# Kernel optimization log

Hardware: AMD Instinct MI355X
Metric: run time of the kernel (lower is better)

The kernel has to match this reference:

```python
import jax, jax.numpy as jnp
import numpy as np

N, D, H, L = 2048, 768, 12, 3
WL, DPE, E = 8, 16, 32768
DFF = 4 * D
EPS = 1e-5


def _ln(x, g, b):
    m = jnp.mean(x, axis=-1, keepdims=True)
    v = jnp.mean(jnp.square(x - m), axis=-1, keepdims=True)
    return (x - m) * jax.lax.rsqrt(v + EPS) * g + b


def setup_inputs() -> dict:
    key = jax.random.key(0)
    ks = jax.random.split(key, 20)
    s = 0.02
    return {
        "node_features": jax.random.normal(ks[0], (N, D), jnp.float32),
        "edge_index": jax.random.randint(ks[1], (2, E), 0, N, jnp.int32),
        "W_rwpe": jax.random.normal(ks[2], (WL, DPE), jnp.float32) * s,
        "b_rwpe": jnp.zeros((DPE,), jnp.float32),
        "Wqkv": jax.random.normal(ks[3], (L, D, 3 * D), jnp.float32) * s,
        "bqkv": jnp.zeros((L, 3 * D), jnp.float32),
        "Wpe": jax.random.normal(ks[4], (L, DPE, H), jnp.float32) * s,
        "bpe": jnp.zeros((L, H), jnp.float32),
        "Wout": jax.random.normal(ks[5], (L, D, D), jnp.float32) * s,
        "bout": jnp.zeros((L, D), jnp.float32),
        "W1": jax.random.normal(ks[6], (L, D, DFF), jnp.float32) * s,
        "b1": jnp.zeros((L, DFF), jnp.float32),
        "W2": jax.random.normal(ks[7], (L, DFF, D), jnp.float32) * s,
        "b2": jnp.zeros((L, D), jnp.float32),
        "g1": jnp.ones((L, D), jnp.float32),
        "beta1": jnp.zeros((L, D), jnp.float32),
        "g2": jnp.ones((L, D), jnp.float32),
        "beta2": jnp.zeros((L, D), jnp.float32),
    }


def _rw_pe(edge_index, W_rwpe, b_rwpe):
    # symmetrized adjacency with duplicate-edge summation (matches coalesce)
    src, tgt = edge_index[0], edge_index[1]
    rows = jnp.concatenate([src, tgt])
    cols = jnp.concatenate([tgt, src])
    A = jnp.zeros((N, N), jnp.float32).at[rows, cols].add(1.0)
    deg = jnp.clip(jnp.sum(A, axis=1), 1.0, None)
    T = A / deg[:, None]
    diags = []
    Tk = T
    for k in range(WL):
        diags.append(jnp.diagonal(Tk))
        if k < WL - 1:
            Tk = Tk @ T
    rw = jnp.stack(diags, axis=1)  # [N, WL]
    return rw @ W_rwpe + b_rwpe  # [N, DPE]


def _forward(node_features, edge_index, W_rwpe, b_rwpe, Wqkv, bqkv, Wpe, bpe,
             Wout, bout, W1, b1, W2, b2, g1, beta1, g2, beta2):
    pe = _rw_pe(edge_index, W_rwpe, b_rwpe)
    hd = D // H
    scale = hd ** -0.5
    h = node_features
    for l in range(L):
        qkv = (h @ Wqkv[l] + bqkv[l]).reshape(N, 3, H, hd)
        q, k, v = qkv[:, 0], qkv[:, 1], qkv[:, 2]  # [N, H, hd]
        pp = pe @ Wpe[l] + bpe[l]  # [N, H]
        # bias[h_, i, j] = pp[j, h_] - pp[i, h_]
        bias = (pp[None, :, :] - pp[:, None, :]).transpose(2, 0, 1)
        scores = jnp.einsum('ihd,jhd->hij', q, k) * scale + bias
        attn = jax.nn.softmax(scores, axis=-1)
        out = jnp.einsum('hij,jhd->ihd', attn, v).reshape(N, D)
        out = out @ Wout[l] + bout[l]
        h = _ln(h + out, g1[l], beta1[l])
        f = jax.nn.gelu(h @ W1[l] + b1[l], approximate=False) @ W2[l] + b2[l]
        h = _ln(h + f, g2[l], beta2[l])
    return h


def reference(node_features, edge_index, W_rwpe, b_rwpe, Wqkv, bqkv, Wpe, bpe,
              Wout, bout, W1, b1, W2, b2, g1, beta1, g2, beta2):
    return _forward(node_features, edge_index, W_rwpe, b_rwpe, Wqkv, bqkv,
                    Wpe, bpe, Wout, bout, W1, b1, W2, b2, g1, beta1, g2, beta2)
```

## Files before the change

kernel.cpp:

```cpp
#include <hip/hip_runtime.h>
#include <math.h>

#define NN 2048
#define EE 32768
#define CAP 256

typedef __attribute__((ext_vector_type(8))) short bf16x8;
typedef __attribute__((ext_vector_type(4))) float f32x4;
typedef __attribute__((ext_vector_type(8))) unsigned short u16x8;
typedef __attribute__((ext_vector_type(4))) unsigned short u16x4;

__device__ inline unsigned short f2bu(float x){
  unsigned u = __builtin_bit_cast(unsigned, x);
  return (unsigned short)((u + 0x7fffu + ((u>>16)&1u)) >> 16);
}
__device__ inline float bu2f(unsigned short h){
  unsigned u = ((unsigned)h) << 16;
  return __builtin_bit_cast(float, u);
}
__device__ inline int swz8(int row, int kg){ return row*32 + ((kg ^ ((row>>1)&3))<<3); }
__device__ inline int swzA(int row, int kg){ return row*64 + ((kg ^ (row&7))<<3); }


__global__ __launch_bounds__(256) void scatter_edges(const int* __restrict__ ei, float* __restrict__ A){
  int e = blockIdx.x*256 + threadIdx.x;
  if (e >= EE) return;
  int s = ei[e], t = ei[EE + e];
  atomicAdd(&A[(size_t)s*NN + t], 1.0f);
  atomicAdd(&A[(size_t)t*NN + s], 1.0f);
}

__global__ __launch_bounds__(256) void row_norm(float* __restrict__ A, float* __restrict__ rw){
  __shared__ float sbuf[4];
  int i = blockIdx.x, t = threadIdx.x;
  float s = 0.f;
  for (int m = t; m < NN; m += 256) s += A[(size_t)i*NN + m];
  for (int w = 32; w >= 1; w >>= 1) s += __shfl_xor(s, w, 64);
  if ((t & 63) == 0) sbuf[t >> 6] = s;
  __syncthreads();
  s = sbuf[0] + sbuf[1] + sbuf[2] + sbuf[3];
  float inv = 1.0f / fmaxf(s, 1.0f);
  for (int m = t; m < NN; m += 256){
    float v = A[(size_t)i*NN + m] * inv;
    A[(size_t)i*NN + m] = v;
    if (m == i) rw[i*8 + 0] = v;
  }
}

__global__ __launch_bounds__(256) void build_csc(const float* __restrict__ T, float* __restrict__ cscv,
                                                 int* __restrict__ cscm, int* __restrict__ cnt){
  __shared__ int scnt;
  int j = blockIdx.x, t = threadIdx.x;
  if (t == 0) scnt = 0;
  __syncthreads();
  for (int m = t; m < NN; m += 256){
    float tv = T[(size_t)j*NN + m];
    if (tv != 0.f){
      int p = atomicAdd(&scnt, 1);
      if (p < CAP){
        cscm[j*CAP + p] = m;
        cscv[j*CAP + p] = T[(size_t)m*NN + j];
      }
    }
  }
  __syncthreads();
  if (t == 0) cnt[j] = min(scnt, CAP);
}

__global__ __launch_bounds__(256) void spmm4(const float* __restrict__ Tk, const float* __restrict__ cscv,
                                             const int* __restrict__ cscm, const int* __restrict__ cnt,
                                             float* __restrict__ Tn, float* __restrict__ rw, int kidx){
  __shared__ float tk[4][NN + 4];
  int i0 = blockIdx.x*4, t = threadIdx.x;
  for (int r = 0; r < 4; r++){
    for (int m4 = t; m4 < NN/4; m4 += 256){
      float4 v = *(const float4*)&Tk[(size_t)(i0+r)*NN + m4*4];
      tk[r][m4*4+0] = v.x; tk[r][m4*4+1] = v.y; tk[r][m4*4+2] = v.z; tk[r][m4*4+3] = v.w;
    }
  }
  __syncthreads();
  for (int j = t; j < NN; j += 256){
    int n = cnt[j];
    const int*   im = &cscm[j*CAP];
    const float* iv = &cscv[j*CAP];
    float a0=0.f,a1=0.f,a2=0.f,a3=0.f;
    for (int c = 0; c < n; c++){
      int m = im[c]; float v = iv[c];
      a0 += v*tk[0][m]; a1 += v*tk[1][m]; a2 += v*tk[2][m]; a3 += v*tk[3][m];
    }
    Tn[(size_t)(i0+0)*NN + j] = a0;
    Tn[(size_t)(i0+1)*NN + j] = a1;
    Tn[(size_t)(i0+2)*NN + j] = a2;
    Tn[(size_t)(i0+3)*NN + j] = a3;
    if (j == i0+0) rw[j*8 + kidx] = a0;
    if (j == i0+1) rw[j*8 + kidx] = a1;
    if (j == i0+2) rw[j*8 + kidx] = a2;
    if (j == i0+3) rw[j*8 + kidx] = a3;
  }
}

__global__ __launch_bounds__(256) void pe_kernel(const float* __restrict__ rw, const float* __restrict__ W,
                                                 const float* __restrict__ b, float* __restrict__ pe){
  int idx = blockIdx.x*256 + threadIdx.x;
  if (idx >= NN*16) return;
  int i = idx >> 4, c = idx & 15;
  float acc = b[c];
  #pragma unroll
  for (int k = 0; k < 8; k++) acc += rw[i*8+k] * W[k*16+c];
  pe[idx] = acc;
}

__global__ __launch_bounds__(256) void pp_kernel(const float* __restrict__ pe, const float* __restrict__ Wpe,
                                                 const float* __restrict__ bpe, float* __restrict__ pp){
  int idx = blockIdx.x*256 + threadIdx.x;
  if (idx >= 3*NN*12) return;
  int l = idx / (NN*12);
  int rm = idx % (NN*12);
  int j = rm / 12, h = rm % 12;
  float acc = bpe[l*12 + h];
  #pragma unroll
  for (int c = 0; c < 16; c++) acc += pe[j*16+c] * Wpe[(l*16+c)*12 + h];
  pp[idx] = acc;
}

__global__ __launch_bounds__(256) void wconv(const float* __restrict__ W, unsigned short* __restrict__ Thi,
                                             unsigned short* __restrict__ Tlo, int K, int N){
  __shared__ float ld[32*33];
  int k0 = blockIdx.y*32, n0 = blockIdx.x*32;
  int t = threadIdx.x;
  int r = t>>3, c4 = (t&7)*4;
  float4 v = *(const float4*)&W[(size_t)(k0+r)*N + n0 + c4];
  ld[(c4+0)*33 + r] = v.x; ld[(c4+1)*33 + r] = v.y; ld[(c4+2)*33 + r] = v.z; ld[(c4+3)*33 + r] = v.w;
  __syncthreads();
  u16x4 hi, lo;
  #pragma unroll
  for (int i = 0; i < 4; i++){
    float x = ld[r*33 + c4 + i];
    unsigned short hh = f2bu(x);
    hi[i] = hh;
    lo[i] = f2bu(x - bu2f(hh));
  }
  *(u16x4*)&Thi[(size_t)(n0+r)*K + k0 + c4] = hi;
  *(u16x4*)&Tlo[(size_t)(n0+r)*K + k0 + c4] = lo;
}

template<int DOGELU, int MREP, int NREP>
__global__ __launch_bounds__(256) void gemm_mfma(const float* __restrict__ A,
    const unsigned short* __restrict__ BThi, const unsigned short* __restrict__ BTlo,
    const float* __restrict__ bias, float* __restrict__ C, int N, int K){
  constexpr int BM = MREP*32, BN = NREP*32;
  constexpr int APT = BM*32/256;
  constexpr int BPT = BN*32/256;
  __shared__ __align__(16) unsigned short smem[(2*BM + 2*BN)*32];
  unsigned short* sAhi = smem;
  unsigned short* sAlo = smem + BM*32;
  unsigned short* sBhi = smem + 2*BM*32;
  unsigned short* sBlo = smem + 2*BM*32 + BN*32;
  const int t = threadIdx.x;
  const int bm = blockIdx.y*BM, bn = blockIdx.x*BN;
  const int lane = t & 63;
  const int wv = t >> 6;
  const int mbase = (wv>>1)*(MREP*16), nbase = (wv&1)*(NREP*16);
  const int lr = lane & 15, kg = lane >> 4;
  f32x4 acc[MREP][NREP];
  #pragma unroll
  for (int m = 0; m < MREP; m++)
    #pragma unroll
    for (int n = 0; n < NREP; n++) acc[m][n] = (f32x4){0.f,0.f,0.f,0.f};

  int arow, akb, brow, bkb;
  if constexpr (BM == 128){ arow = t>>1; akb = (t&1)*16; } else { arow = t>>2; akb = (t&3)*8; }
  if constexpr (BN == 128){ brow = t>>1; bkb = (t&1)*16; } else { brow = t>>2; bkb = (t&3)*8; }

  for (int k0 = 0; k0 < K; k0 += 32){
    float fa[APT];
    unsigned short fbh[BPT], fbl[BPT];
    const float* pA = &A[(size_t)(bm+arow)*K + k0 + akb];
    #pragma unroll
    for (int i = 0; i < APT/4; i++) *(float4*)&fa[i*4] = *(const float4*)&pA[i*4];
    const unsigned short* pBh = &BThi[(size_t)(bn+brow)*K + k0 + bkb];
    const unsigned short* pBl = &BTlo[(size_t)(bn+brow)*K + k0 + bkb];
    #pragma unroll
    for (int i = 0; i < BPT/8; i++){
      *(u16x8*)&fbh[i*8] = *(const u16x8*)&pBh[i*8];
      *(u16x8*)&fbl[i*8] = *(const u16x8*)&pBl[i*8];
    }
    __syncthreads();
    #pragma unroll
    for (int g = 0; g < APT/8; g++){
      u16x8 hi, lo;
      #pragma unroll
      for (int j = 0; j < 8; j++){
        float x = fa[g*8+j];
        unsigned short hh = f2bu(x);
        hi[j] = hh;
        lo[j] = f2bu(x - bu2f(hh));
      }
      int kgw = (akb>>3) + g;
      *(u16x8*)&sAhi[swz8(arow, kgw)] = hi;
      *(u16x8*)&sAlo[swz8(arow, kgw)] = lo;
    }
    #pragma unroll
    for (int g = 0; g < BPT/8; g++){
      int kgw = (bkb>>3) + g;
      *(u16x8*)&sBhi[swz8(brow, kgw)] = *(u16x8*)&fbh[g*8];
      *(u16x8*)&sBlo[swz8(brow, kgw)] = *(u16x8*)&fbl[g*8];
    }
    __syncthreads();
    bf16x8 ah[MREP], al[MREP], bh[NREP], bl[NREP];
    #pragma unroll
    for (int m = 0; m < MREP; m++){
      int o = swz8(mbase + m*16 + lr, kg);
      ah[m] = *(bf16x8*)&sAhi[o];
      al[m] = *(bf16x8*)&sAlo[o];
    }
    #pragma unroll
    for (int n = 0; n < NREP; n++){
      int o = swz8(nbase + n*16 + lr, kg);
      bh[n] = *(bf16x8*)&sBhi[o];
      bl[n] = *(bf16x8*)&sBlo[o];
    }
    #pragma unroll
    for (int m = 0; m < MREP; m++)
      #pragma unroll
      for (int n = 0; n < NREP; n++){
        acc[m][n] = __builtin_amdgcn_mfma_f32_16x16x32_bf16(ah[m], bh[n], acc[m][n], 0, 0, 0);
        acc[m][n] = __builtin_amdgcn_mfma_f32_16x16x32_bf16(al[m], bh[n], acc[m][n], 0, 0, 0);
        acc[m][n] = __builtin_amdgcn_mfma_f32_16x16x32_bf16(ah[m], bl[n], acc[m][n], 0, 0, 0);
      }
  }
  #pragma unroll
  for (int m = 0; m < MREP; m++)
    #pragma unroll
    for (int n = 0; n < NREP; n++){
      int col = bn + nbase + n*16 + lr;
      int row0 = bm + mbase + m*16 + kg*4;
      float bb = bias[col];
      #pragma unroll
      for (int j = 0; j < 4; j++){
        float o = acc[m][n][j] + bb;
        if (DOGELU) o = 0.5f*o*(1.f + erff(o*0.70710678118f));
        C[(size_t)(row0+j)*N + col] = o;
      }
    }
}

__global__ __launch_bounds__(256) void qkv_planes(const float* __restrict__ qkv,
    unsigned short* __restrict__ qhi, unsigned short* __restrict__ qlo,
    unsigned short* __restrict__ khi, unsigned short* __restrict__ klo,
    unsigned short* __restrict__ vthi, unsigned short* __restrict__ vtlo){
  __shared__ float vb[64*69];
  const int h = blockIdx.y, j0 = blockIdx.x*64;
  const int t = threadIdx.x;
  const int jl = t >> 4, d4 = (t & 15)*4;
  #pragma unroll
  for (int p = 0; p < 4; p++){
    int j = jl + p*16;
    const float* row = &qkv[(size_t)(j0 + j)*2304 + h*64 + d4];
    float4 q4 = *(const float4*)&row[0];
    float4 k4 = *(const float4*)&row[768];
    float4 v4 = *(const float4*)&row[1536];
    float qv[4] = {q4.x*0.125f, q4.y*0.125f, q4.z*0.125f, q4.w*0.125f};
    float kv[4] = {k4.x, k4.y, k4.z, k4.w};
    float vv[4] = {v4.x, v4.y, v4.z, v4.w};
    u16x4 qh_, ql_, kh_, kl_;
    #pragma unroll
    for (int i = 0; i < 4; i++){
      unsigned short hh = f2bu(qv[i]); qh_[i] = hh; ql_[i] = f2bu(qv[i] - bu2f(hh));
      hh = f2bu(kv[i]); kh_[i] = hh; kl_[i] = f2bu(kv[i] - bu2f(hh));
      vb[(d4+i)*0 + j*69 + d4 + i] = vv[i];
    }
    size_t ob = ((size_t)h*NN + j0 + j)*64 + d4;
    *(u16x4*)&qhi[ob] = qh_; *(u16x4*)&qlo[ob] = ql_;
    *(u16x4*)&khi[ob] = kh_; *(u16x4*)&klo[ob] = kl_;
  }
  __syncthreads();
  #pragma unroll
  for (int p = 0; p < 4; p++){
    int d = jl + p*16;
    u16x4 vh_, vl_;
    #pragma unroll
    for (int i = 0; i < 4; i++){
      float x = vb[(d4+i)*69 + d];
      unsigned short hh = f2bu(x);
      vh_[i] = hh; vl_[i] = f2bu(x - bu2f(hh));
    }
    size_t ob = ((size_t)h*64 + d)*NN + j0 + d4;
    *(u16x4*)&vthi[ob] = vh_;
    *(u16x4*)&vtlo[ob] = vl_;
  }
}

__global__ __launch_bounds__(256) void attn_mfma(
    const unsigned short* __restrict__ qhi, const unsigned short* __restrict__ qlo,
    const unsigned short* __restrict__ khi, const unsigned short* __restrict__ klo,
    const unsigned short* __restrict__ vthi, const unsigned short* __restrict__ vtlo,
    const float* __restrict__ pp, float* __restrict__ opart,
    float* __restrict__ mbuf, float* __restrict__ lbuf){
  __shared__ __align__(16) unsigned short sKhi[64*64], sKlo[64*64];
  __shared__ __align__(16) unsigned short sVhi[64*64], sVlo[64*64];
  __shared__ __align__(16) unsigned short sPhi[64*64], sPlo[64*64];
  __shared__ float ppj[64];
  const int h = blockIdx.y, i0 = blockIdx.x*64, z = blockIdx.z;
  const int t = threadIdx.x, l = t & 63, w = t >> 6;
  const int lr = l & 15, lg = l >> 4;
  const int q0w = w*16;
  const int qrow = i0 + q0w + lr;
  bf16x8 qh[2], ql[2];
  #pragma unroll
  for (int ks = 0; ks < 2; ks++){
    size_t qo = ((size_t)h*NN + qrow)*64 + (ks*4 + lg)*8;
    qh[ks] = *(const bf16x8*)&qhi[qo];
    ql[ks] = *(const bf16x8*)&qlo[qo];
  }
  float mrow = -1e30f, lrow = 0.f;
  f32x4 oacc[4];
  #pragma unroll
  for (int dt = 0; dt < 4; dt++) oacc[dt] = (f32x4){0.f,0.f,0.f,0.f};

  for (int jt = 0; jt < 16; jt++){
    const int jb = z*(NN/2) + jt*64;
    __syncthreads();
    {
      size_t kb = ((size_t)h*NN + jb + l)*64;
      size_t vbg = ((size_t)h*64 + l)*NN + jb;
      #pragma unroll
      for (int i = 0; i < 2; i++){
        int dg = w*2 + i;
        *(u16x8*)&sKhi[swzA(l, dg)] = *(const u16x8*)&khi[kb + dg*8];
        *(u16x8*)&sKlo[swzA(l, dg)] = *(const u16x8*)&klo[kb + dg*8];
        *(u16x8*)&sVhi[swzA(l, dg)] = *(const u16x8*)&vthi[vbg + dg*8];
        *(u16x8*)&sVlo[swzA(l, dg)] = *(const u16x8*)&vtlo[vbg + dg*8];
      }
      if (t < 64) ppj[t] = pp[(size_t)(jb + t)*12 + h];
    }
    __syncthreads();
    f32x4 sa[4];
    #pragma unroll
    for (int j4 = 0; j4 < 4; j4++) sa[j4] = (f32x4){0.f,0.f,0.f,0.f};
    #pragma unroll
    for (int j4 = 0; j4 < 4; j4++){
      #pragma unroll
      for (int ks = 0; ks < 2; ks++){
        int ro = j4*16 + lr, dg = ks*4 + lg;
        bf16x8 kh = *(const bf16x8*)&sKhi[swzA(ro, dg)];
        bf16x8 kl = *(const bf16x8*)&sKlo[swzA(ro, dg)];
        sa[j4] = __builtin_amdgcn_mfma_f32_16x16x32_bf16(kh, qh[ks], sa[j4], 0, 0, 0);
        sa[j4] = __builtin_amdgcn_mfma_f32_16x16x32_bf16(kl, qh[ks], sa[j4], 0, 0, 0);
        sa[j4] = __builtin_amdgcn_mfma_f32_16x16x32_bf16(kh, ql[ks], sa[j4], 0, 0, 0);
      }
    }
    float mx = -1e30f;
    #pragma unroll
    for (int j4 = 0; j4 < 4; j4++)
      #pragma unroll
      for (int r = 0; r < 4; r++){
        sa[j4][r] += ppj[j4*16 + lg*4 + r];
        mx = fmaxf(mx, sa[j4][r]);
      }
    mx = fmaxf(mx, __shfl_xor(mx, 16, 64));
    mx = fmaxf(mx, __shfl_xor(mx, 32, 64));
    float mn = fmaxf(mrow, mx);
    float alq = expf(mrow - mn);
    mrow = mn;
    float rs = 0.f;
    #pragma unroll
    for (int j4 = 0; j4 < 4; j4++)
      #pragma unroll
      for (int r = 0; r < 4; r++){
        float pv = expf(sa[j4][r] - mn);
        sa[j4][r] = pv;
        rs += pv;
      }
    rs += __shfl_xor(rs, 16, 64);
    rs += __shfl_xor(rs, 32, 64);
    lrow = lrow*alq + rs;
    #pragma unroll
    for (int dt = 0; dt < 4; dt++)
      #pragma unroll
      for (int r = 0; r < 4; r++) oacc[dt][r] *= alq;
    #pragma unroll
    for (int j4 = 0; j4 < 4; j4++)
      #pragma unroll
      for (int r = 0; r < 4; r++){
        int j = j4*16 + lg*4 + r, q = q0w + lr;
        int o = q*64 + (((j>>3) ^ (q&7))<<3) + (j&7);
        float pv = sa[j4][r];
        unsigned short ph = f2bu(pv);
        sPhi[o] = ph;
        sPlo[o] = f2bu(pv - bu2f(ph));
      }
    #pragma unroll
    for (int ks = 0; ks < 2; ks++){
      int q = q0w + lr, dg = ks*4 + lg;
      bf16x8 pf = *(const bf16x8*)&sPhi[swzA(q, dg)];
      bf16x8 pl = *(const bf16x8*)&sPlo[swzA(q, dg)];
      #pragma unroll
      for (int dt = 0; dt < 4; dt++){
        int dr = dt*16 + lr;
        bf16x8 vh = *(const bf16x8*)&sVhi[swzA(dr, dg)];
        bf16x8 vl = *(const bf16x8*)&sVlo[swzA(dr, dg)];
        oacc[dt] = __builtin_amdgcn_mfma_f32_16x16x32_bf16(vh, pf, oacc[dt], 0, 0, 0);
        oacc[dt] = __builtin_amdgcn_mfma_f32_16x16x32_bf16(vh, pl, oacc[dt], 0, 0, 0);
        oacc[dt] = __builtin_amdgcn_mfma_f32_16x16x32_bf16(vl, pf, oacc[dt], 0, 0, 0);
      }
    }
  }
  #pragma unroll
  for (int dt = 0; dt < 4; dt++)
    #pragma unroll
    for (int r = 0; r < 4; r++){
      int d = dt*16 + lg*4 + r;
      opart[(((size_t)z*NN + qrow)*12 + h)*64 + d] = oacc[dt][r];
    }
  if (lg == 0){
    mbuf[((size_t)z*NN + qrow)*12 + h] = mrow;
    lbuf[((size_t)z*NN + qrow)*12 + h] = lrow;
  }
}

__global__ __launch_bounds__(256) void attn_merge(const float* __restrict__ opart, const float* __restrict__ mbuf,
                                                  const float* __restrict__ lbuf, float* __restrict__ outp){
  int idx = blockIdx.x*256 + threadIdx.x;
  int ih = idx >> 6;
  int q = ih / 12, hh = ih % 12, d = idx & 63;
  float m0 = mbuf[ih], m1 = mbuf[NN*12 + ih];
  float l0 = lbuf[ih], l1 = lbuf[NN*12 + ih];
  float mm = fmaxf(m0, m1);
  float e0 = expf(m0 - mm), e1 = expf(m1 - mm);
  float L = l0*e0 + l1*e1;
  float o = (opart[idx]*e0 + opart[(size_t)NN*12*64 + idx]*e1) / L;
  outp[(size_t)q*768 + hh*64 + d] = o;
}

__global__ __launch_bounds__(256) void add_ln(const float* __restrict__ X, const float* __restrict__ R,
                                              const float* __restrict__ g, const float* __restrict__ b,
                                              float* __restrict__ Y){
  __shared__ float sbuf[4];
  int i = blockIdx.x, t = threadIdx.x;
  float x0 = X[(size_t)i*768 + t]       + R[(size_t)i*768 + t];
  float x1 = X[(size_t)i*768 + t + 256] + R[(size_t)i*768 + t + 256];
  float x2 = X[(size_t)i*768 + t + 512] + R[(size_t)i*768 + t + 512];
  float s = x0 + x1 + x2;
  for (int w = 32; w >= 1; w >>= 1) s += __shfl_xor(s, w, 64);
  if ((t & 63) == 0) sbuf[t >> 6] = s;
  __syncthreads();
  s = sbuf[0] + sbuf[1] + sbuf[2] + sbuf[3];
  float mean = s * (1.0f/768.0f);
  float d0 = x0-mean, d1 = x1-mean, d2 = x2-mean;
  float vv = d0*d0 + d1*d1 + d2*d2;
  __syncthreads();
  for (int w = 32; w >= 1; w >>= 1) vv += __shfl_xor(vv, w, 64);
  if ((t & 63) == 0) sbuf[t >> 6] = vv;
  __syncthreads();
  vv = sbuf[0] + sbuf[1] + sbuf[2] + sbuf[3];
  float inv = 1.0f / sqrtf(vv*(1.0f/768.0f) + 1e-5f);
  Y[(size_t)i*768 + t]       = d0*inv*g[t]     + b[t];
  Y[(size_t)i*768 + t + 256] = d1*inv*g[t+256] + b[t+256];
  Y[(size_t)i*768 + t + 512] = d2*inv*g[t+512] + b[t+512];
}

extern "C" void kernel_launch(void* const* d_in, const int* in_sizes, int n_in,
                              void* d_out, int out_size, void* d_ws, size_t ws_size,
                              hipStream_t stream) {
  const float* nf     = (const float*)d_in[0];
  const int*   ei     = (const int*)  d_in[1];
  const float* W_rwpe = (const float*)d_in[2];
  const float* b_rwpe = (const float*)d_in[3];
  const float* Wqkv   = (const float*)d_in[4];
  const float* bqkv   = (const float*)d_in[5];
  const float* Wpe    = (const float*)d_in[6];
  const float* bpe    = (const float*)d_in[7];
  const float* Wout   = (const float*)d_in[8];
  const float* bout   = (const float*)d_in[9];
  const float* W1     = (const float*)d_in[10];
  const float* b1     = (const float*)d_in[11];
  const float* W2     = (const float*)d_in[12];
  const float* b2     = (const float*)d_in[13];
  const float* g1     = (const float*)d_in[14];
  const float* be1    = (const float*)d_in[15];
  const float* g2     = (const float*)d_in[16];
  const float* be2    = (const float*)d_in[17];
  float* out = (float*)d_out;
  (void)in_sizes; (void)n_in; (void)out_size; (void)ws_size;

  char* base = (char*)d_ws;
  size_t off = 0;
  auto alloc = [&](size_t bytes){ void* p = base + off; off += (bytes + 255) & ~(size_t)255; return p; };

  const size_t PL = 7077888ULL;
  const size_t oQ = 0, oO = 1769472ULL, oW1 = 2359296ULL, oW2 = 4718592ULL;
  unsigned short* whi = (unsigned short*)alloc(3*PL*2);
  unsigned short* wlo = (unsigned short*)alloc(3*PL*2);
  float* rw  = (float*)alloc((size_t)NN*8*4);
  float* pe  = (float*)alloc((size_t)NN*16*4);
  float* pp  = (float*)alloc((size_t)3*NN*12*4);
  char*  U   = (char*)alloc(93000000ULL);

  float* P0   = (float*)U;
  float* P1   = P0 + (size_t)NN*NN;
  float* cscv = P1 + (size_t)NN*NN;
  int*   cscm = (int*)(cscv + (size_t)NN*CAP);
  int*   cnt  = (int*)(cscm + (size_t)NN*CAP);
  float* qkvb  = (float*)U;
  float* attnb = qkvb  + (size_t)NN*2304;
  float* projb = attnb + (size_t)NN*768;
  float* h1    = projb + (size_t)NN*768;
  float* ffn1  = h1    + (size_t)NN*768;
  float* ffn2  = ffn1  + (size_t)NN*3072;
  float* hb    = ffn2  + (size_t)NN*768;
  float* opart = hb    + (size_t)NN*768;
  float* mbuf  = opart + (size_t)2*NN*12*64;
  float* lbuf  = mbuf  + (size_t)2*NN*12;
  const size_t PS = (size_t)12*NN*64;
  unsigned short* qhi_p = (unsigned short*)ffn1;
  unsigned short* qlo_p = qhi_p + PS;
  unsigned short* khi_p = qhi_p + 2*PS;
  unsigned short* klo_p = qhi_p + 3*PS;
  unsigned short* vthi_p = qhi_p + 4*PS;
  unsigned short* vtlo_p = qhi_p + 5*PS;

  for (int l = 0; l < 3; l++){
    wconv<<<dim3(2304/32, 768/32), 256, 0, stream>>>(Wqkv + (size_t)l*768*2304, whi + l*PL + oQ,  wlo + l*PL + oQ,  768, 2304);
    wconv<<<dim3(768/32,  768/32), 256, 0, stream>>>(Wout + (size_t)l*768*768,  whi + l*PL + oO,  wlo + l*PL + oO,  768, 768);
    wconv<<<dim3(3072/32, 768/32), 256, 0, stream>>>(W1   + (size_t)l*768*3072, whi + l*PL + oW1, wlo + l*PL + oW1, 768, 3072);
    wconv<<<dim3(768/32, 3072/32), 256, 0, stream>>>(W2   + (size_t)l*3072*768, whi + l*PL + oW2, wlo + l*PL + oW2, 3072, 768);
  }

  hipMemsetAsync(P0, 0, (size_t)NN*NN*4, stream);
  scatter_edges<<<EE/256, 256, 0, stream>>>(ei, P0);
  row_norm<<<NN, 256, 0, stream>>>(P0, rw);
  build_csc<<<NN, 256, 0, stream>>>(P0, cscv, cscm, cnt);
  for (int k = 1; k < 8; k++){
    const float* src = (k & 1) ? P0 : P1;
    float*       dst = (k & 1) ? P1 : P0;
    spmm4<<<NN/4, 256, 0, stream>>>(src, cscv, cscm, cnt, dst, rw, k);
  }
  pe_kernel<<<NN*16/256, 256, 0, stream>>>(rw, W_rwpe, b_rwpe, pe);
  pp_kernel<<<3*NN*12/256, 256, 0, stream>>>(pe, Wpe, bpe, pp);

  const float* h = nf;
  for (int l = 0; l < 3; l++){
    gemm_mfma<0,4,4><<<dim3(2304/128, 2048/128), 256, 0, stream>>>(h, whi + l*PL + oQ, wlo + l*PL + oQ, bqkv + (size_t)l*2304, qkvb, 2304, 768);
    qkv_planes<<<dim3(NN/64, 12), 256, 0, stream>>>(qkvb, qhi_p, qlo_p, khi_p, klo_p, vthi_p, vtlo_p);
    attn_mfma<<<dim3(NN/64, 12, 2), 256, 0, stream>>>(qhi_p, qlo_p, khi_p, klo_p, vthi_p, vtlo_p,
                                                      pp + (size_t)l*NN*12, opart, mbuf, lbuf);
    attn_merge<<<NN*12*64/256, 256, 0, stream>>>(opart, mbuf, lbuf, attnb);
    gemm_mfma<0,2,2><<<dim3(768/64, 2048/64), 256, 0, stream>>>(attnb, whi + l*PL + oO, wlo + l*PL + oO, bout + (size_t)l*768, projb, 768, 768);
    add_ln<<<NN, 256, 0, stream>>>(projb, h, g1 + (size_t)l*768, be1 + (size_t)l*768, h1);
    gemm_mfma<1,4,4><<<dim3(3072/128, 2048/128), 256, 0, stream>>>(h1, whi + l*PL + oW1, wlo + l*PL + oW1, b1 + (size_t)l*3072, ffn1, 3072, 768);
    gemm_mfma<0,2,2><<<dim3(768/64, 2048/64), 256, 0, stream>>>(ffn1, whi + l*PL + oW2, wlo + l*PL + oW2, b2 + (size_t)l*768, ffn2, 768, 3072);
    float* hout = (l == 2) ? out : hb;
    add_ln<<<NN, 256, 0, stream>>>(ffn2, h1, g2 + (size_t)l*768, be2 + (size_t)l*768, hout);
    h = hout;
  }
}
```

Measured before the change: 1.473 ms.

## Pre-split GEMM activations into bf16 hi/lo planes and simplify attention softmax

```diff
diff --git a/kernel.cpp b/kernel.cpp
--- a/kernel.cpp
+++ b/kernel.cpp
@@ -4,6 +4,7 @@
 #define NN 2048
 #define EE 32768
 #define CAP 256
+#define LOG2E 1.4426950408889634f
 
 typedef __attribute__((ext_vector_type(8))) short bf16x8;
 typedef __attribute__((ext_vector_type(4))) float f32x4;
@@ -144,13 +145,31 @@
   *(u16x4*)&Tlo[(size_t)(n0+r)*K + k0 + c4] = lo;
 }
 
+__global__ __launch_bounds__(256) void split_planes(const float* __restrict__ X,
+    unsigned short* __restrict__ Hi, unsigned short* __restrict__ Lo, int n4){
+  int i = blockIdx.x*256 + threadIdx.x;
+  if (i >= n4) return;
+  float4 v = ((const float4*)X)[i];
+  float xs[4] = {v.x, v.y, v.z, v.w};
+  u16x4 hi, lo;
+  #pragma unroll
+  for (int k = 0; k < 4; k++){
+    unsigned short hh = f2bu(xs[k]);
+    hi[k] = hh; lo[k] = f2bu(xs[k] - bu2f(hh));
+  }
+  ((u16x4*)Hi)[i] = hi;
+  ((u16x4*)Lo)[i] = lo;
+}
+
 template<int DOGELU, int MREP, int NREP>
-__global__ __launch_bounds__(256) void gemm_mfma(const float* __restrict__ A,
+__global__ __launch_bounds__(256) void gemm_mfma(
+    const unsigned short* __restrict__ Ahi, const unsigned short* __restrict__ Alo,
     const unsigned short* __restrict__ BThi, const unsigned short* __restrict__ BTlo,
-    const float* __restrict__ bias, float* __restrict__ C, int N, int K){
+    const float* __restrict__ bias, float* __restrict__ C,
+    unsigned short* __restrict__ Chi, unsigned short* __restrict__ Clo, int N, int K){
   constexpr int BM = MREP*32, BN = NREP*32;
-  constexpr int APT = BM*32/256;
-  constexpr int BPT = BN*32/256;
+  constexpr int APT8 = BM*32/256/8;
+  constexpr int BPT8 = BN*32/256/8;
   __shared__ __align__(16) unsigned short smem[(2*BM + 2*BN)*32];
   unsigned short* sAhi = smem;
   unsigned short* sAlo = smem + BM*32;
@@ -173,38 +192,33 @@
   if constexpr (BN == 128){ brow = t>>1; bkb = (t&1)*16; } else { brow = t>>2; bkb = (t&3)*8; }
 
   for (int k0 = 0; k0 < K; k0 += 32){
-    float fa[APT];
-    unsigned short fbh[BPT], fbl[BPT];
-    const float* pA = &A[(size_t)(bm+arow)*K + k0 + akb];
-    #pragma unroll
-    for (int i = 0; i < APT/4; i++) *(float4*)&fa[i*4] = *(const float4*)&pA[i*4];
+    u16x8 fah[APT8], fal[APT8], fbh[BPT8], fbl[BPT8];
+    const unsigned short* pAh = &Ahi[(size_t)(bm+arow)*K + k0 + akb];
+    const unsigned short* pAl = &Alo[(size_t)(bm+arow)*K + k0 + akb];
+    #pragma unroll
+    for (int i = 0; i < APT8; i++){
+      fah[i] = *(const u16x8*)&pAh[i*8];
+      fal[i] = *(const u16x8*)&pAl[i*8];
+    }
     const unsigned short* pBh = &BThi[(size_t)(bn+brow)*K + k0 + bkb];
     const unsigned short* pBl = &BTlo[(size_t)(bn+brow)*K + k0 + bkb];
     #pragma unroll
-    for (int i = 0; i < BPT/8; i++){
-      *(u16x8*)&fbh[i*8] = *(const u16x8*)&pBh[i*8];
-      *(u16x8*)&fbl[i*8] = *(const u16x8*)&pBl[i*8];
+    for (int i = 0; i < BPT8; i++){
+      fbh[i] = *(const u16x8*)&pBh[i*8];
+      fbl[i] = *(const u16x8*)&pBl[i*8];
     }
     __syncthreads();
     #pragma unroll
-    for (int g = 0; g < APT/8; g++){
-      u16x8 hi, lo;
-      #pragma unroll
-      for (int j = 0; j < 8; j++){
-        float x = fa[g*8+j];
-        unsigned short hh = f2bu(x);
-        hi[j] = hh;
-        lo[j] = f2bu(x - bu2f(hh));
-      }
+    for (int g = 0; g < APT8; g++){
       int kgw = (akb>>3) + g;
-      *(u16x8*)&sAhi[swz8(arow, kgw)] = hi;
-      *(u16x8*)&sAlo[swz8(arow, kgw)] = lo;
-    }
-    #pragma unroll
-    for (int g = 0; g < BPT/8; g++){
+      *(u16x8*)&sAhi[swz8(arow, kgw)] = fah[g];
+      *(u16x8*)&sAlo[swz8(arow, kgw)] = fal[g];
+    }
+    #pragma unroll
+    for (int g = 0; g < BPT8; g++){
       int kgw = (bkb>>3) + g;
-      *(u16x8*)&sBhi[swz8(brow, kgw)] = *(u16x8*)&fbh[g*8];
-      *(u16x8*)&sBlo[swz8(brow, kgw)] = *(u16x8*)&fbl[g*8];
+      *(u16x8*)&sBhi[swz8(brow, kgw)] = fbh[g];
+      *(u16x8*)&sBlo[swz8(brow, kgw)] = fbl[g];
     }
     __syncthreads();
     bf16x8 ah[MREP], al[MREP], bh[NREP], bl[NREP];
@@ -239,8 +253,15 @@
       #pragma unroll
       for (int j = 0; j < 4; j++){
         float o = acc[m][n][j] + bb;
-        if (DOGELU) o = 0.5f*o*(1.f + erff(o*0.70710678118f));
-        C[(size_t)(row0+j)*N + col] = o;
+        size_t idx = (size_t)(row0+j)*N + col;
+        if constexpr (DOGELU){
+          o = 0.5f*o*(1.f + erff(o*0.70710678118f));
+          unsigned short hh = f2bu(o);
+          Chi[idx] = hh;
+          Clo[idx] = f2bu(o - bu2f(hh));
+        } else {
+          C[idx] = o;
+        }
       }
     }
 }
@@ -253,6 +274,7 @@
   const int h = blockIdx.y, j0 = blockIdx.x*64;
   const int t = threadIdx.x;
   const int jl = t >> 4, d4 = (t & 15)*4;
+  const float qsc = 0.125f * LOG2E;
   #pragma unroll
   for (int p = 0; p < 4; p++){
     int j = jl + p*16;
@@ -260,7 +282,7 @@
     float4 q4 = *(const float4*)&row[0];
     float4 k4 = *(const float4*)&row[768];
     float4 v4 = *(const float4*)&row[1536];
-    float qv[4] = {q4.x*0.125f, q4.y*0.125f, q4.z*0.125f, q4.w*0.125f};
+    float qv[4] = {q4.x*qsc, q4.y*qsc, q4.z*qsc, q4.w*qsc};
     float kv[4] = {k4.x, k4.y, k4.z, k4.w};
     float vv[4] = {v4.x, v4.y, v4.z, v4.w};
     u16x4 qh_, ql_, kh_, kl_;
@@ -268,7 +290,7 @@
     for (int i = 0; i < 4; i++){
       unsigned short hh = f2bu(qv[i]); qh_[i] = hh; ql_[i] = f2bu(qv[i] - bu2f(hh));
       hh = f2bu(kv[i]); kh_[i] = hh; kl_[i] = f2bu(kv[i] - bu2f(hh));
-      vb[(d4+i)*0 + j*69 + d4 + i] = vv[i];
+      vb[j*69 + d4 + i] = vv[i];
     }
     size_t ob = ((size_t)h*NN + j0 + j)*64 + d4;
     *(u16x4*)&qhi[ob] = qh_; *(u16x4*)&qlo[ob] = ql_;
@@ -299,8 +321,8 @@
     float* __restrict__ mbuf, float* __restrict__ lbuf){
   __shared__ __align__(16) unsigned short sKhi[64*64], sKlo[64*64];
   __shared__ __align__(16) unsigned short sVhi[64*64], sVlo[64*64];
-  __shared__ __align__(16) unsigned short sPhi[64*64], sPlo[64*64];
   __shared__ float ppj[64];
+  unsigned short* sP = sKhi;
   const int h = blockIdx.y, i0 = blockIdx.x*64, z = blockIdx.z;
   const int t = threadIdx.x, l = t & 63, w = t >> 6;
   const int lr = l & 15, lg = l >> 4;
@@ -332,7 +354,7 @@
         *(u16x8*)&sVhi[swzA(l, dg)] = *(const u16x8*)&vthi[vbg + dg*8];
         *(u16x8*)&sVlo[swzA(l, dg)] = *(const u16x8*)&vtlo[vbg + dg*8];
       }
-      if (t < 64) ppj[t] = pp[(size_t)(jb + t)*12 + h];
+      if (t < 64) ppj[t] = pp[(size_t)(jb + t)*12 + h] * LOG2E;
     }
     __syncthreads();
     f32x4 sa[4];
@@ -361,14 +383,14 @@
     mx = fmaxf(mx, __shfl_xor(mx, 16, 64));
     mx = fmaxf(mx, __shfl_xor(mx, 32, 64));
     float mn = fmaxf(mrow, mx);
-    float alq = expf(mrow - mn);
+    float alq = __builtin_amdgcn_exp2f(mrow - mn);
     mrow = mn;
     float rs = 0.f;
     #pragma unroll
     for (int j4 = 0; j4 < 4; j4++)
       #pragma unroll
       for (int r = 0; r < 4; r++){
-        float pv = expf(sa[j4][r] - mn);
+        float pv = __builtin_amdgcn_exp2f(sa[j4][r] - mn);
         sa[j4][r] = pv;
         rs += pv;
       }
@@ -379,29 +401,29 @@
     for (int dt = 0; dt < 4; dt++)
       #pragma unroll
       for (int r = 0; r < 4; r++) oacc[dt][r] *= alq;
-    #pragma unroll
-    for (int j4 = 0; j4 < 4; j4++)
-      #pragma unroll
-      for (int r = 0; r < 4; r++){
-        int j = j4*16 + lg*4 + r, q = q0w + lr;
-        int o = q*64 + (((j>>3) ^ (q&7))<<3) + (j&7);
-        float pv = sa[j4][r];
-        unsigned short ph = f2bu(pv);
-        sPhi[o] = ph;
-        sPlo[o] = f2bu(pv - bu2f(ph));
-      }
+    __syncthreads();
+    {
+      int q = q0w + lr;
+      #pragma unroll
+      for (int j4 = 0; j4 < 4; j4++){
+        int jgrp = j4*2 + (lg>>1);
+        int o = q*64 + ((jgrp ^ (q&7))<<3) + (lg&1)*4;
+        u16x4 pk;
+        #pragma unroll
+        for (int r = 0; r < 4; r++) pk[r] = f2bu(sa[j4][r]);
+        *(u16x4*)&sP[o] = pk;
+      }
+    }
     #pragma unroll
     for (int ks = 0; ks < 2; ks++){
       int q = q0w + lr, dg = ks*4 + lg;
-      bf16x8 pf = *(const bf16x8*)&sPhi[swzA(q, dg)];
-      bf16x8 pl = *(const bf16x8*)&sPlo[swzA(q, dg)];
+      bf16x8 pf = *(const bf16x8*)&sP[swzA(q, dg)];
       #pragma unroll
       for (int dt = 0; dt < 4; dt++){
         int dr = dt*16 + lr;
         bf16x8 vh = *(const bf16x8*)&sVhi[swzA(dr, dg)];
         bf16x8 vl = *(const bf16x8*)&sVlo[swzA(dr, dg)];
         oacc[dt] = __builtin_amdgcn_mfma_f32_16x16x32_bf16(vh, pf, oacc[dt], 0, 0, 0);
-        oacc[dt] = __builtin_amdgcn_mfma_f32_16x16x32_bf16(vh, pl, oacc[dt], 0, 0, 0);
         oacc[dt] = __builtin_amdgcn_mfma_f32_16x16x32_bf16(vl, pf, oacc[dt], 0, 0, 0);
       }
     }
@@ -420,22 +442,29 @@
 }
 
 __global__ __launch_bounds__(256) void attn_merge(const float* __restrict__ opart, const float* __restrict__ mbuf,
-                                                  const float* __restrict__ lbuf, float* __restrict__ outp){
+                                                  const float* __restrict__ lbuf,
+                                                  unsigned short* __restrict__ outHi,
+                                                  unsigned short* __restrict__ outLo){
   int idx = blockIdx.x*256 + threadIdx.x;
   int ih = idx >> 6;
   int q = ih / 12, hh = ih % 12, d = idx & 63;
   float m0 = mbuf[ih], m1 = mbuf[NN*12 + ih];
   float l0 = lbuf[ih], l1 = lbuf[NN*12 + ih];
   float mm = fmaxf(m0, m1);
-  float e0 = expf(m0 - mm), e1 = expf(m1 - mm);
+  float e0 = __builtin_amdgcn_exp2f(m0 - mm), e1 = __builtin_amdgcn_exp2f(m1 - mm);
   float L = l0*e0 + l1*e1;
   float o = (opart[idx]*e0 + opart[(size_t)NN*12*64 + idx]*e1) / L;
-  outp[(size_t)q*768 + hh*64 + d] = o;
+  size_t oi = (size_t)q*768 + hh*64 + d;
+  unsigned short hb_ = f2bu(o);
+  outHi[oi] = hb_;
+  outLo[oi] = f2bu(o - bu2f(hb_));
 }
 
 __global__ __launch_bounds__(256) void add_ln(const float* __restrict__ X, const float* __restrict__ R,
                                               const float* __restrict__ g, const float* __restrict__ b,
-                                              float* __restrict__ Y){
+                                              float* __restrict__ Y,
+                                              unsigned short* __restrict__ Yhi,
+                                              unsigned short* __restrict__ Ylo){
   __shared__ float sbuf[4];
   int i = blockIdx.x, t = threadIdx.x;
   float x0 = X[(size_t)i*768 + t]       + R[(size_t)i*768 + t];
@@ -455,9 +484,15 @@
   __syncthreads();
   vv = sbuf[0] + sbuf[1] + sbuf[2] + sbuf[3];
   float inv = 1.0f / sqrtf(vv*(1.0f/768.0f) + 1e-5f);
-  Y[(size_t)i*768 + t]       = d0*inv*g[t]     + b[t];
-  Y[(size_t)i*768 + t + 256] = d1*inv*g[t+256] + b[t+256];
-  Y[(size_t)i*768 + t + 512] = d2*inv*g[t+512] + b[t+512];
+  float y0 = d0*inv*g[t]     + b[t];
+  float y1 = d1*inv*g[t+256] + b[t+256];
+  float y2 = d2*inv*g[t+512] + b[t+512];
+  size_t base = (size_t)i*768 + t;
+  Y[base] = y0; Y[base+256] = y1; Y[base+512] = y2;
+  unsigned short hh;
+  hh = f2bu(y0); Yhi[base]     = hh; Ylo[base]     = f2bu(y0 - bu2f(hh));
+  hh = f2bu(y1); Yhi[base+256] = hh; Ylo[base+256] = f2bu(y1 - bu2f(hh));
+  hh = f2bu(y2); Yhi[base+512] = hh; Ylo[base+512] = f2bu(y2 - bu2f(hh));
 }
 
 extern "C" void kernel_launch(void* const* d_in, const int* in_sizes, int n_in,
@@ -495,25 +530,31 @@
   float* rw  = (float*)alloc((size_t)NN*8*4);
   float* pe  = (float*)alloc((size_t)NN*16*4);
   float* pp  = (float*)alloc((size_t)3*NN*12*4);
-  char*  U   = (char*)alloc(93000000ULL);
+  char*  U   = (char*)alloc(92000000ULL);
 
   float* P0   = (float*)U;
   float* P1   = P0 + (size_t)NN*NN;
   float* cscv = P1 + (size_t)NN*NN;
   int*   cscm = (int*)(cscv + (size_t)NN*CAP);
   int*   cnt  = (int*)(cscm + (size_t)NN*CAP);
-  float* qkvb  = (float*)U;
-  float* attnb = qkvb  + (size_t)NN*2304;
-  float* projb = attnb + (size_t)NN*768;
-  float* h1    = projb + (size_t)NN*768;
-  float* ffn1  = h1    + (size_t)NN*768;
-  float* ffn2  = ffn1  + (size_t)NN*3072;
-  float* hb    = ffn2  + (size_t)NN*768;
-  float* opart = hb    + (size_t)NN*768;
-  float* mbuf  = opart + (size_t)2*NN*12*64;
-  float* lbuf  = mbuf  + (size_t)2*NN*12;
-  const size_t PS = (size_t)12*NN*64;
-  unsigned short* qhi_p = (unsigned short*)ffn1;
+  float* qkvb    = (float*)U;
+  float* opart   = qkvb;
+  float* mbuf    = qkvb + (size_t)2*NN*12*64;
+  float* lbuf    = mbuf + (size_t)2*NN*12;
+  unsigned short* attnbHi = (unsigned short*)(qkvb + (size_t)NN*2304);
+  unsigned short* attnbLo = attnbHi + (size_t)NN*768;
+  float* projb   = (float*)(attnbLo + (size_t)NN*768);
+  float* h1      = projb + (size_t)NN*768;
+  unsigned short* h1hi = (unsigned short*)(h1 + (size_t)NN*768);
+  unsigned short* h1lo = h1hi + (size_t)NN*768;
+  unsigned short* f1hi = h1lo + (size_t)NN*768;
+  unsigned short* f1lo = f1hi + (size_t)NN*3072;
+  float* ffn2    = (float*)(f1lo + (size_t)NN*3072);
+  float* hb      = ffn2 + (size_t)NN*768;
+  unsigned short* hbhi = (unsigned short*)(hb + (size_t)NN*768);
+  unsigned short* hblo = hbhi + (size_t)NN*768;
+  const size_t PS = (size_t)NN*768;
+  unsigned short* qhi_p = f1hi;
   unsigned short* qlo_p = qhi_p + PS;
   unsigned short* khi_p = qhi_p + 2*PS;
   unsigned short* klo_p = qhi_p + 3*PS;
@@ -539,19 +580,21 @@
   pe_kernel<<<NN*16/256, 256, 0, stream>>>(rw, W_rwpe, b_rwpe, pe);
   pp_kernel<<<3*NN*12/256, 256, 0, stream>>>(pe, Wpe, bpe, pp);
 
-  const float* h = nf;
+  split_planes<<<(NN*768/4 + 255)/256, 256, 0, stream>>>(nf, hbhi, hblo, NN*768/4);
+
+  const float* hres = nf;
   for (int l = 0; l < 3; l++){
-    gemm_mfma<0,4,4><<<dim3(2304/128, 2048/128), 256, 0, stream>>>(h, whi + l*PL + oQ, wlo + l*PL + oQ, bqkv + (size_t)l*2304, qkvb, 2304, 768);
+    gemm_mfma<0,4,4><<<dim3(2304/128, 2048/128), 256, 0, stream>>>(hbhi, hblo, whi + l*PL + oQ, wlo + l*PL + oQ, bqkv + (size_t)l*2304, qkvb, nullptr, nullptr, 2304, 768);
     qkv_planes<<<dim3(NN/64, 12), 256, 0, stream>>>(qkvb, qhi_p, qlo_p, khi_p, klo_p, vthi_p, vtlo_p);
     attn_mfma<<<dim3(NN/64, 12, 2), 256, 0, stream>>>(qhi_p, qlo_p, khi_p, klo_p, vthi_p, vtlo_p,
                                                       pp + (size_t)l*NN*12, opart, mbuf, lbuf);
-    attn_merge<<<NN*12*64/256, 256, 0, stream>>>(opart, mbuf, lbuf, attnb);
-    gemm_mfma<0,2,2><<<dim3(768/64, 2048/64), 256, 0, stream>>>(attnb, whi + l*PL + oO, wlo + l*PL + oO, bout + (size_t)l*768, projb, 768, 768);
-    add_ln<<<NN, 256, 0, stream>>>(projb, h, g1 + (size_t)l*768, be1 + (size_t)l*768, h1);
-    gemm_mfma<1,4,4><<<dim3(3072/128, 2048/128), 256, 0, stream>>>(h1, whi + l*PL + oW1, wlo + l*PL + oW1, b1 + (size_t)l*3072, ffn1, 3072, 768);
-    gemm_mfma<0,2,2><<<dim3(768/64, 2048/64), 256, 0, stream>>>(ffn1, whi + l*PL + oW2, wlo + l*PL + oW2, b2 + (size_t)l*768, ffn2, 768, 3072);
+    attn_merge<<<NN*12*64/256, 256, 0, stream>>>(opart, mbuf, lbuf, attnbHi, attnbLo);
+    gemm_mfma<0,2,2><<<dim3(768/64, 2048/64), 256, 0, stream>>>(attnbHi, attnbLo, whi + l*PL + oO, wlo + l*PL + oO, bout + (size_t)l*768, projb, nullptr, nullptr, 768, 768);
+    add_ln<<<NN, 256, 0, stream>>>(projb, hres, g1 + (size_t)l*768, be1 + (size_t)l*768, h1, h1hi, h1lo);
+    gemm_mfma<1,4,4><<<dim3(3072/128, 2048/128), 256, 0, stream>>>(h1hi, h1lo, whi + l*PL + oW1, wlo + l*PL + oW1, b1 + (size_t)l*3072, nullptr, f1hi, f1lo, 3072, 768);
+    gemm_mfma<0,2,2><<<dim3(768/64, 2048/64), 256, 0, stream>>>(f1hi, f1lo, whi + l*PL + oW2, wlo + l*PL + oW2, b2 + (size_t)l*768, ffn2, nullptr, nullptr, 768, 3072);
     float* hout = (l == 2) ? out : hb;
-    add_ln<<<NN, 256, 0, stream>>>(ffn2, h1, g2 + (size_t)l*768, be2 + (size_t)l*768, hout);
-    h = hout;
-  }
-}
+    add_ln<<<NN, 256, 0, stream>>>(ffn2, h1, g2 + (size_t)l*768, be2 + (size_t)l*768, hout, hbhi, hblo);
+    hres = hb;
+  }
+}
```

Result: faster. 1.400 ms (-5.0%).
